# Optimization experiments

Hardware: AMD Instinct MI355X
Metric: run time of the kernel (lower is better)

The kernel has to match this reference:

```python
import jax, jax.numpy as jnp
import numpy as np

NUM_GROUPS = 32
EPS = 1e-5


def setup_inputs() -> dict:
    key = jax.random.key(0)
    ks = jax.random.split(key, 11)
    B, C, H, W = 4, 512, 64, 64
    s = 1.0 / np.sqrt(C)
    inp = {
        "x": jax.random.normal(ks[0], (B, C, H, W), dtype=jnp.float32),
        "gn_w": jnp.ones((C,), jnp.float32),
        "gn_b": jnp.zeros((C,), jnp.float32),
        "wq": jax.random.uniform(ks[1], (C, C), jnp.float32, -s, s),
        "bq": jax.random.uniform(ks[2], (C,), jnp.float32, -s, s),
        "wk": jax.random.uniform(ks[3], (C, C), jnp.float32, -s, s),
        "bk": jax.random.uniform(ks[4], (C,), jnp.float32, -s, s),
        "wv": jax.random.uniform(ks[5], (C, C), jnp.float32, -s, s),
        "bv": jax.random.uniform(ks[6], (C,), jnp.float32, -s, s),
        "wo": jax.random.uniform(ks[7], (C, C), jnp.float32, -s, s),
        "bo": jax.random.uniform(ks[8], (C,), jnp.float32, -s, s),
    }
    return inp


def reference(x, gn_w, gn_b, wq, bq, wk, bk, wv, bv, wo, bo):
    B, C, H, W = x.shape
    HW = H * W
    # GroupNorm(32, C)
    g = x.reshape(B, NUM_GROUPS, C // NUM_GROUPS, H, W)
    mu = jnp.mean(g, axis=(2, 3, 4), keepdims=True)
    var = jnp.var(g, axis=(2, 3, 4), keepdims=True)
    h = ((g - mu) * jax.lax.rsqrt(var + EPS)).reshape(B, C, H, W)
    h = h * gn_w[None, :, None, None] + gn_b[None, :, None, None]
    # Faithful to original: .view (reshape), NOT permute -> (B, HW, C)
    h = h.reshape(B, HW, C)
    q = h @ wq.T + bq  # (B, HW, C)
    k = h @ wk.T + bk
    v = h @ wv.T + bv
    # Faithful: reshape (not transpose) to (B, C, HW)
    q = q.reshape(B, C, HW)
    k = k.reshape(B, C, HW)
    v = v.reshape(B, C, HW)
    # attn: (B, HW, HW)
    attn = jnp.einsum('bcn,bcm->bnm', q, k)
    attn = jax.nn.softmax(attn, axis=-1)
    # out: (B, C, HW) = v @ attn^T
    out = jnp.einsum('bcm,bnm->bcn', v, attn)
    # transpose to (B, HW, C), out-proj, then reshape back
    out = jnp.swapaxes(out, 1, 2) @ wo.T + bo
    out = out.reshape(B, C, H, W)
    return out + x
```

## Files before the change

### kernel.cpp

```cpp
#include <hip/hip_runtime.h>
#include <hip/hip_fp16.h>
#include <math.h>

constexpr int BATCH = 4;
constexpr int HWDIM = 4096;
constexpr long CNT   = 2097152;
constexpr long ACNT  = 16777216;
constexpr int GSIZE = 65536;
constexpr float GN_EPS = 1e-5f;

typedef __attribute__((ext_vector_type(8))) _Float16 f16x8;
typedef __attribute__((ext_vector_type(4))) float f32x4;

__device__ __forceinline__ unsigned pkf16(float a, float b) {
  __half ha = __float2half(a), hb = __float2half(b);
  return (unsigned)__half_as_ushort(ha) | ((unsigned)__half_as_ushort(hb) << 16);
}
__device__ __forceinline__ float2 up2(unsigned u) {
  __half2 h = *(__half2*)&u;
  return __half22float2(h);
}
__device__ __forceinline__ void gl_lds16(const void* g, void* l) {
  __builtin_amdgcn_global_load_lds((const __attribute__((address_space(1))) unsigned*)g,
                                   (__attribute__((address_space(3))) unsigned*)l, 16, 0, 0);
}

__global__ void gn_stats_kernel(const float* __restrict__ x,
                                float* __restrict__ mu, float* __restrict__ rs) {
  const int grp = blockIdx.x;
  const float4* p = (const float4*)(x + (long)grp * GSIZE);
  float s = 0.f, q = 0.f;
  for (int i = threadIdx.x; i < GSIZE / 4; i += 256) {
    float4 v = p[i];
    s += (v.x + v.y) + (v.z + v.w);
    q += (v.x * v.x + v.y * v.y) + (v.z * v.z + v.w * v.w);
  }
  #pragma unroll
  for (int o = 32; o > 0; o >>= 1) { s += __shfl_xor(s, o, 64); q += __shfl_xor(q, o, 64); }
  __shared__ float ls[4], lq[4];
  if ((threadIdx.x & 63) == 0) { ls[threadIdx.x >> 6] = s; lq[threadIdx.x >> 6] = q; }
  __syncthreads();
  if (threadIdx.x == 0) {
    float S = (ls[0] + ls[1]) + (ls[2] + ls[3]);
    float Q = (lq[0] + lq[1]) + (lq[2] + lq[3]);
    float m = S * (1.f / GSIZE);
    float var = Q * (1.f / GSIZE) - m * m;
    mu[grp] = m; rs[grp] = rsqrtf(var + GN_EPS);
  }
}

__global__ void gn_norm_f16(const float* __restrict__ x,
                            const float* __restrict__ mu, const float* __restrict__ rs,
                            const float* __restrict__ gw, const float* __restrict__ gb,
                            unsigned short* __restrict__ h) {
  long i = ((long)blockIdx.x * 256 + threadIdx.x) * 4;
  int c   = (int)((i >> 12) & 511);
  int grp = (int)(i >> 16);
  float m = mu[grp], r = rs[grp];
  float w = gw[c] * r;
  float bia = gb[c] - m * w;
  float4 v = *(const float4*)(x + i);
  *(uint2*)(h + i) = (uint2){ pkf16(v.x * w + bia, v.y * w + bia),
                              pkf16(v.z * w + bia, v.w * w + bia) };
}

__global__ void wcvt(const float* __restrict__ w0, const float* __restrict__ w1,
                     const float* __restrict__ w2, const float* __restrict__ w3,
                     unsigned short* __restrict__ o) {
  const float* src = blockIdx.y == 0 ? w0 : blockIdx.y == 1 ? w1 : blockIdx.y == 2 ? w2 : w3;
  long e = ((long)blockIdx.x * 256 + threadIdx.x) * 4;
  float4 v = *(const float4*)(src + e);
  *(uint2*)(o + (long)blockIdx.y * 262144 + e) = (uint2){ pkf16(v.x, v.y), pkf16(v.z, v.w) };
}

template<int K>
__device__ __forceinline__ void gemm_core(const unsigned short* __restrict__ Ab, long sA,
                                          const unsigned short* __restrict__ Bb, long sB,
                                          unsigned short* LB, const int t, f32x4 (&acc)[4][4]) {
  const int lane = t & 63, w = t >> 6, wm = w & 1, wn = w >> 1;

  auto stage = [&](int buf, int k0) {
    unsigned short* S = LB + buf * 16384;
    #pragma unroll
    for (int fbi = 0; fbi < 4; fbi++) {
      int fb = w * 4 + fbi;
      int row = (fb >> 1) * 16 + (lane & 15);
      int g   = (fb & 1) * 4 + (lane >> 4);
      gl_lds16(Ab + (long)row * sA + k0 + g * 8, &S[(fb * 64) << 3]);
      gl_lds16(Bb + (long)row * sB + k0 + g * 8, &S[8192 + ((fb * 64) << 3)]);
    }
  };
  auto compute = [&](int buf) {
    const unsigned short* As = LB + buf * 16384;
    const unsigned short* Bs = As + 8192;
    #pragma unroll
    for (int kk = 0; kk < 2; kk++) {
      f16x8 a[4], b[4];
      #pragma unroll
      for (int i = 0; i < 4; i++)
        a[i] = *(const f16x8*)&As[(((wm * 4 + i) * 2 + kk) * 64 + lane) << 3];
      #pragma unroll
      for (int j = 0; j < 4; j++)
        b[j] = *(const f16x8*)&Bs[(((wn * 4 + j) * 2 + kk) * 64 + lane) << 3];
      #pragma unroll
      for (int i = 0; i < 4; i++)
        #pragma unroll
        for (int j = 0; j < 4; j++)
          acc[i][j] = __builtin_amdgcn_mfma_f32_16x16x32_f16(a[i], b[j], acc[i][j], 0, 0, 0);
    }
  };

  stage(0, 0);
  stage(1, 64);
  asm volatile("s_waitcnt vmcnt(8)" ::: "memory");
  __builtin_amdgcn_s_barrier();
  __builtin_amdgcn_sched_barrier(0);

  #pragma unroll 1
  for (int k0 = 0; k0 + 192 <= K; k0 += 64) {
    const int cur = (k0 >> 6) & 1;
    compute(cur);
    __builtin_amdgcn_sched_barrier(0);
    __builtin_amdgcn_s_barrier();
    stage(cur, k0 + 128);
    asm volatile("s_waitcnt vmcnt(8)" ::: "memory");
    __builtin_amdgcn_s_barrier();
    __builtin_amdgcn_sched_barrier(0);
  }
  compute(((K - 128) >> 6) & 1);
  asm volatile("s_waitcnt vmcnt(0)" ::: "memory");
  __builtin_amdgcn_s_barrier();
  __builtin_amdgcn_sched_barrier(0);
  compute(((K - 64) >> 6) & 1);
  __syncthreads();
}

__launch_bounds__(256)
__global__ void proj_qkv(const unsigned short* __restrict__ A, const unsigned short* __restrict__ WF,
                         const float* __restrict__ bq, const float* __restrict__ bk,
                         const float* __restrict__ bv, unsigned short* __restrict__ outq) {
  __shared__ __align__(16) unsigned short LB[32768];
  const int z = blockIdx.z;
  const unsigned short* W = WF + (long)z * 262144;
  const float* bias = z == 0 ? bq : z == 1 ? bk : bv;
  unsigned short* outp = outq + (long)z * 8388608;
  const int m0 = blockIdx.x * 128, n0 = blockIdx.y * 128;
  const int t = threadIdx.x;

  f32x4 acc[4][4];
  #pragma unroll
  for (int i = 0; i < 4; i++)
    #pragma unroll
    for (int j = 0; j < 4; j++) acc[i][j] = (f32x4){0.f, 0.f, 0.f, 0.f};

  gemm_core<512>(A + (long)m0 * 512, 512, W + (long)n0 * 512, 512, LB, t, acc);

  const int lane = t & 63, w = t >> 6, wm = w & 1, wn = w >> 1;
  const int lm = lane & 15, quad = lane >> 4;
  #pragma unroll
  for (int i = 0; i < 4; i++)
    #pragma unroll
    for (int j = 0; j < 4; j++) {
      int rr = wm * 64 + i * 16 + quad * 4;
      int cc = wn * 64 + j * 16 + lm;
      float bb = bias[n0 + cc];
      #pragma unroll
      for (int r = 0; r < 4; r++)
        LB[(rr + r) * 136 + cc] = __half_as_ushort(__float2half(acc[i][j][r] + bb));
    }
  __syncthreads();
  #pragma unroll
  for (int k = 0; k < 8; k++) {
    int ro = k * 16 + (t >> 4), col = (t & 15) * 8;
    uint4 vv = *(const uint4*)&LB[ro * 136 + col];
    *(uint4*)(outp + (long)(m0 + ro) * 512 + n0 + col) = vv;
  }
}

__launch_bounds__(256)
__global__ void proj_out(const unsigned short* __restrict__ A, const unsigned short* __restrict__ W,
                         const float* __restrict__ bias, const float* __restrict__ res,
                         float* __restrict__ outv) {
  __shared__ __align__(16) unsigned short LB[32768];
  const int m0 = blockIdx.x * 128, n0 = blockIdx.y * 128;
  const int t = threadIdx.x;

  f32x4 acc[4][4];
  #pragma unroll
  for (int i = 0; i < 4; i++)
    #pragma unroll
    for (int j = 0; j < 4; j++) acc[i][j] = (f32x4){0.f, 0.f, 0.f, 0.f};

  gemm_core<512>(A + (long)m0 * 512, 512, W + (long)n0 * 512, 512, LB, t, acc);

  const int lane = t & 63, w = t >> 6, wm = w & 1, wn = w >> 1;
  const int lm = lane & 15, quad = lane >> 4;
  #pragma unroll
  for (int i = 0; i < 4; i++)
    #pragma unroll
    for (int j = 0; j < 4; j++) {
      int nn = m0 + wm * 64 + i * 16 + quad * 4;
      int cc = n0 + wn * 64 + j * 16 + lm;
      float bb = bias[cc];
      #pragma unroll
      for (int r = 0; r < 4; r++) {
        long idx = (long)(nn + r) * 512 + cc;
        outv[idx] = acc[i][j][r] + bb + res[idx];
      }
    }
}

__global__ void transpose_f16(const unsigned short* __restrict__ qb,
                              const unsigned short* __restrict__ kb,
                              unsigned short* __restrict__ tr) {
  __shared__ __align__(16) unsigned short ld[64 * 72];
  const int zb = blockIdx.z;
  const int b = zb >> 1;
  const unsigned short* in = (zb & 1 ? kb : qb) + (long)b * CNT;
  unsigned short* o = tr + (long)b * 2 * CNT + (zb & 1 ? CNT : 0);
  const int n0 = blockIdx.x * 64, c0 = blockIdx.y * 64;
  const int t = threadIdx.x;
  unsigned* ld32 = (unsigned*)ld;
  {
    const int p = t >> 3, cg = t & 7;
    uint4 r0 = *(const uint4*)(in + (long)(c0 + 2 * p) * 4096 + n0 + 8 * cg);
    uint4 r1 = *(const uint4*)(in + (long)(c0 + 2 * p + 1) * 4096 + n0 + 8 * cg);
    unsigned aw[4] = { r0.x, r0.y, r0.z, r0.w };
    unsigned bw[4] = { r1.x, r1.y, r1.z, r1.w };
    #pragma unroll
    for (int i = 0; i < 4; i++) {
      ld32[(8 * cg + 2 * i) * 36 + p]     = (aw[i] & 0xFFFFu) | (bw[i] << 16);
      ld32[(8 * cg + 2 * i + 1) * 36 + p] = (aw[i] >> 16) | (bw[i] & 0xFFFF0000u);
    }
  }
  __syncthreads();
  {
    const int n = t >> 2, cg2 = t & 3;
    uint4 o0 = *(const uint4*)(ld + n * 72 + 16 * cg2);
    uint4 o1 = *(const uint4*)(ld + n * 72 + 16 * cg2 + 8);
    *(uint4*)(o + (long)(n0 + n) * 512 + c0 + 16 * cg2)     = o0;
    *(uint4*)(o + (long)(n0 + n) * 512 + c0 + 16 * cg2 + 8) = o1;
  }
}

__launch_bounds__(256)
__global__ void qk_f16(const unsigned short* __restrict__ tr, unsigned short* __restrict__ attn) {
  __shared__ __align__(16) unsigned short LB[32768];
  const int lin = blockIdx.x + 32 * blockIdx.y + 1024 * blockIdx.z;
  const int nl = (lin & 7) * 512 + (lin >> 3);
  const int b = nl >> 10, by = (nl >> 5) & 31, bx = nl & 31;
  const unsigned short* qT = tr + (long)b * 2 * CNT;
  const unsigned short* kT = qT + CNT;
  unsigned short* attnb = attn + (long)b * ACNT;
  const int n0 = bx * 128, m0 = by * 128;
  const int t = threadIdx.x;

  f32x4 acc[4][4];
  #pragma unroll
  for (int i = 0; i < 4; i++)
    #pragma unroll
    for (int j = 0; j < 4; j++) acc[i][j] = (f32x4){0.f, 0.f, 0.f, 0.f};

  gemm_core<512>(qT + (long)n0 * 512, 512, kT + (long)m0 * 512, 512, LB, t, acc);

  const int lane = t & 63, w = t >> 6, wm = w & 1, wn = w >> 1;
  const int lm = lane & 15, quad = lane >> 4;
  #pragma unroll
  for (int i = 0; i < 4; i++)
    #pragma unroll
    for (int j = 0; j < 4; j++) {
      int rr = wm * 64 + i * 16 + quad * 4;
      int cc = wn * 64 + j * 16 + lm;
      #pragma unroll
      for (int r = 0; r < 4; r++)
        LB[(rr + r) * 136 + cc] = __half_as_ushort(__float2half(acc[i][j][r]));
    }
  __syncthreads();
  #pragma unroll
  for (int k = 0; k < 8; k++) {
    int ro = k * 16 + (t >> 4), col = (t & 15) * 8;
    uint4 vv = *(const uint4*)&LB[ro * 136 + col];
    *(uint4*)(attnb + (long)(n0 + ro) * 4096 + m0 + col) = vv;
  }
}

__global__ void softmax_f16ip(unsigned short* __restrict__ attn) {
  unsigned short* p = attn + (long)blockIdx.x * HWDIM;
  const int t = threadIdx.x;
  uint4 u0 = *(const uint4*)(p + t * 16);
  uint4 u1 = *(const uint4*)(p + t * 16 + 8);
  float v[16];
  {
    unsigned uu[8] = { u0.x, u0.y, u0.z, u0.w, u1.x, u1.y, u1.z, u1.w };
    #pragma unroll
    for (int i = 0; i < 8; i++) { float2 f = up2(uu[i]); v[2*i] = f.x; v[2*i+1] = f.y; }
  }
  float mx = -1e30f;
  #pragma unroll
  for (int i = 0; i < 16; i++) mx = fmaxf(mx, v[i]);
  #pragma unroll
  for (int o = 32; o > 0; o >>= 1) mx = fmaxf(mx, __shfl_xor(mx, o, 64));
  __shared__ float rmax[4], rsum[4];
  if ((t & 63) == 0) rmax[t >> 6] = mx;
  __syncthreads();
  mx = fmaxf(fmaxf(rmax[0], rmax[1]), fmaxf(rmax[2], rmax[3]));
  float s = 0.f;
  #pragma unroll
  for (int i = 0; i < 16; i++) { v[i] = __expf(v[i] - mx); s += v[i]; }
  #pragma unroll
  for (int o = 32; o > 0; o >>= 1) s += __shfl_xor(s, o, 64);
  if ((t & 63) == 0) rsum[t >> 6] = s;
  __syncthreads();
  s = (rsum[0] + rsum[1]) + (rsum[2] + rsum[3]);
  float inv = 1.f / s;
  uint4 w0, w1;
  w0.x = pkf16(v[0]*inv,  v[1]*inv);  w0.y = pkf16(v[2]*inv,  v[3]*inv);
  w0.z = pkf16(v[4]*inv,  v[5]*inv);  w0.w = pkf16(v[6]*inv,  v[7]*inv);
  w1.x = pkf16(v[8]*inv,  v[9]*inv);  w1.y = pkf16(v[10]*inv, v[11]*inv);
  w1.z = pkf16(v[12]*inv, v[13]*inv); w1.w = pkf16(v[14]*inv, v[15]*inv);
  *(uint4*)(p + t * 16)     = w0;
  *(uint4*)(p + t * 16 + 8) = w1;
}

__launch_bounds__(256)
__global__ void pv_f16(const unsigned short* __restrict__ P, const unsigned short* __restrict__ V,
                       unsigned short* __restrict__ ot) {
  __shared__ __align__(16) unsigned short LB[32768];
  const int lin = blockIdx.x + 32 * blockIdx.y + 128 * blockIdx.z;
  const int nl = (lin & 7) * 64 + (lin >> 3);
  const int bx = nl & 31, by = (nl >> 5) & 3, b = nl >> 7;
  const unsigned short* Pb = P + (long)b * ACNT;
  const unsigned short* Vb = V + (long)b * CNT;
  unsigned short* Ob = ot + (long)b * CNT;
  const int n0 = bx * 128, c0 = by * 128;
  const int t = threadIdx.x;

  f32x4 acc[4][4];
  #pragma unroll
  for (int i = 0; i < 4; i++)
    #pragma unroll
    for (int j = 0; j < 4; j++) acc[i][j] = (f32x4){0.f, 0.f, 0.f, 0.f};

  gemm_core<4096>(Pb + (long)n0 * 4096, 4096, Vb + (long)c0 * 4096, 4096, LB, t, acc);

  const int lane = t & 63, w = t >> 6, wm = w & 1, wn = w >> 1;
  const int lm = lane & 15, quad = lane >> 4;
  #pragma unroll
  for (int i = 0; i < 4; i++)
    #pragma unroll
    for (int j = 0; j < 4; j++) {
      int rr = wm * 64 + i * 16 + quad * 4;
      int cc = wn * 64 + j * 16 + lm;
      #pragma unroll
      for (int r = 0; r < 4; r++)
        LB[(rr + r) * 136 + cc] = __half_as_ushort(__float2half(acc[i][j][r]));
    }
  __syncthreads();
  #pragma unroll
  for (int k = 0; k < 8; k++) {
    int ro = k * 16 + (t >> 4), col = (t & 15) * 8;
    uint4 vv = *(const uint4*)&LB[ro * 136 + col];
    *(uint4*)(Ob + (long)(n0 + ro) * 512 + c0 + col) = vv;
  }
}

extern "C" void kernel_launch(void* const* d_in, const int* in_sizes, int n_in,
                              void* d_out, int out_size, void* d_ws, size_t ws_size,
                              hipStream_t stream) {
  (void)in_sizes; (void)n_in; (void)out_size; (void)ws_size;
  const float* x  = (const float*)d_in[0];
  const float* gw = (const float*)d_in[1];
  const float* gb = (const float*)d_in[2];
  const float* wq = (const float*)d_in[3];
  const float* bq = (const float*)d_in[4];
  const float* wk = (const float*)d_in[5];
  const float* bk = (const float*)d_in[6];
  const float* wv = (const float*)d_in[7];
  const float* bv = (const float*)d_in[8];
  const float* wo = (const float*)d_in[9];
  const float* bo = (const float*)d_in[10];
  float* out = (float*)d_out;

  unsigned short* attn = (unsigned short*)d_ws;
  unsigned short* h    = attn;
  unsigned short* qf   = attn + 4 * ACNT;
  unsigned short* kf   = qf + 8388608;
  unsigned short* vf   = kf + 8388608;
  unsigned short* tr   = vf + 8388608;
  unsigned short* ot   = tr + 16777216;
  unsigned short* wf   = ot + 8388608;
  float* mu = (float*)(wf + 1048576);
  float* rs = mu + 128;

  gn_stats_kernel<<<dim3(128), dim3(256), 0, stream>>>(x, mu, rs);
  gn_norm_f16<<<dim3(8192), dim3(256), 0, stream>>>(x, mu, rs, gw, gb, h);
  wcvt<<<dim3(256, 4), dim3(256), 0, stream>>>(wq, wk, wv, wo, wf);

  proj_qkv<<<dim3(128, 4, 3), 256, 0, stream>>>(h, wf, bq, bk, bv, qf);

  transpose_f16<<<dim3(64, 8, 8), 256, 0, stream>>>(qf, kf, tr);
  qk_f16<<<dim3(32, 32, 4), 256, 0, stream>>>(tr, attn);
  softmax_f16ip<<<dim3(16384), 256, 0, stream>>>(attn);
  pv_f16<<<dim3(32, 4, 4), 256, 0, stream>>>(attn, vf, ot);

  proj_out<<<dim3(128, 4), 256, 0, stream>>>(ot, wf + 786432, bo, x, out);
}
```

Before: 512.2 us.

## Enlarge GEMM tiles to 256x256 with K=32 stages and split GroupNorm stats

```diff
diff --git a/kernel.cpp b/kernel.cpp
--- a/kernel.cpp
+++ b/kernel.cpp
@@ -24,13 +24,18 @@
   __builtin_amdgcn_global_load_lds((const __attribute__((address_space(1))) unsigned*)g,
                                    (__attribute__((address_space(3))) unsigned*)l, 16, 0, 0);
 }
-
-__global__ void gn_stats_kernel(const float* __restrict__ x,
-                                float* __restrict__ mu, float* __restrict__ rs) {
-  const int grp = blockIdx.x;
-  const float4* p = (const float4*)(x + (long)grp * GSIZE);
+template<int N> __device__ __forceinline__ void wait_vmcnt() {
+  if constexpr (N == 0)      asm volatile("s_waitcnt vmcnt(0)" ::: "memory");
+  else if constexpr (N == 4) asm volatile("s_waitcnt vmcnt(4)" ::: "memory");
+  else if constexpr (N == 6) asm volatile("s_waitcnt vmcnt(6)" ::: "memory");
+}
+
+__global__ void gn_stats_kernel(const float* __restrict__ x, float* __restrict__ sacc) {
+  const int blk = blockIdx.x;
+  const int grp = blk >> 2;
+  const float4* p = (const float4*)(x + (long)grp * GSIZE + (long)(blk & 3) * (GSIZE / 4));
   float s = 0.f, q = 0.f;
-  for (int i = threadIdx.x; i < GSIZE / 4; i += 256) {
+  for (int i = threadIdx.x; i < GSIZE / 16; i += 256) {
     float4 v = p[i];
     s += (v.x + v.y) + (v.z + v.w);
     q += (v.x * v.x + v.y * v.y) + (v.z * v.z + v.w * v.w);
@@ -41,22 +46,20 @@
   if ((threadIdx.x & 63) == 0) { ls[threadIdx.x >> 6] = s; lq[threadIdx.x >> 6] = q; }
   __syncthreads();
   if (threadIdx.x == 0) {
-    float S = (ls[0] + ls[1]) + (ls[2] + ls[3]);
-    float Q = (lq[0] + lq[1]) + (lq[2] + lq[3]);
-    float m = S * (1.f / GSIZE);
-    float var = Q * (1.f / GSIZE) - m * m;
-    mu[grp] = m; rs[grp] = rsqrtf(var + GN_EPS);
-  }
-}
-
-__global__ void gn_norm_f16(const float* __restrict__ x,
-                            const float* __restrict__ mu, const float* __restrict__ rs,
+    atomicAdd(&sacc[grp * 2],     (ls[0] + ls[1]) + (ls[2] + ls[3]));
+    atomicAdd(&sacc[grp * 2 + 1], (lq[0] + lq[1]) + (lq[2] + lq[3]));
+  }
+}
+
+__global__ void gn_norm_f16(const float* __restrict__ x, const float* __restrict__ sacc,
                             const float* __restrict__ gw, const float* __restrict__ gb,
                             unsigned short* __restrict__ h) {
   long i = ((long)blockIdx.x * 256 + threadIdx.x) * 4;
   int c   = (int)((i >> 12) & 511);
   int grp = (int)(i >> 16);
-  float m = mu[grp], r = rs[grp];
+  float S = sacc[grp * 2], Q = sacc[grp * 2 + 1];
+  float m = S * (1.f / GSIZE);
+  float r = rsqrtf(Q * (1.f / GSIZE) - m * m + GN_EPS);
   float w = gw[c] * r;
   float bia = gb[c] - m * w;
   float4 v = *(const float4*)(x + i);
@@ -73,69 +76,108 @@
   *(uint2*)(o + (long)blockIdx.y * 262144 + e) = (uint2){ pkf16(v.x, v.y), pkf16(v.z, v.w) };
 }
 
-template<int K>
+template<int BM, int BN, int NWM, int NWN, int K>
 __device__ __forceinline__ void gemm_core(const unsigned short* __restrict__ Ab, long sA,
                                           const unsigned short* __restrict__ Bb, long sB,
-                                          unsigned short* LB, const int t, f32x4 (&acc)[4][4]) {
+                                          unsigned short* LB, const int t, f32x4 (&acc)[8][4]) {
+  constexpr int NW   = NWM * NWN;
+  constexpr int APW  = BM / 16 / NW;
+  constexpr int BPW  = BN / 16 / NW;
+  constexpr int L    = APW + BPW;
+  constexpr int BUFS = (BM + BN) * 32;
   const int lane = t & 63, w = t >> 6, wm = w & 1, wn = w >> 1;
 
   auto stage = [&](int buf, int k0) {
-    unsigned short* S = LB + buf * 16384;
-    #pragma unroll
-    for (int fbi = 0; fbi < 4; fbi++) {
-      int fb = w * 4 + fbi;
-      int row = (fb >> 1) * 16 + (lane & 15);
-      int g   = (fb & 1) * 4 + (lane >> 4);
-      gl_lds16(Ab + (long)row * sA + k0 + g * 8, &S[(fb * 64) << 3]);
-      gl_lds16(Bb + (long)row * sB + k0 + g * 8, &S[8192 + ((fb * 64) << 3)]);
+    unsigned short* S = LB + buf * BUFS;
+    #pragma unroll
+    for (int i = 0; i < APW; i++) {
+      int fb = w * APW + i;
+      gl_lds16(Ab + (long)(fb * 16 + (lane & 15)) * sA + k0 + (lane >> 4) * 8, &S[fb * 512]);
+    }
+    #pragma unroll
+    for (int i = 0; i < BPW; i++) {
+      int fb = w * BPW + i;
+      gl_lds16(Bb + (long)(fb * 16 + (lane & 15)) * sB + k0 + (lane >> 4) * 8,
+               &S[BM * 32 + fb * 512]);
     }
   };
   auto compute = [&](int buf) {
-    const unsigned short* As = LB + buf * 16384;
-    const unsigned short* Bs = As + 8192;
-    #pragma unroll
-    for (int kk = 0; kk < 2; kk++) {
-      f16x8 a[4], b[4];
-      #pragma unroll
-      for (int i = 0; i < 4; i++)
-        a[i] = *(const f16x8*)&As[(((wm * 4 + i) * 2 + kk) * 64 + lane) << 3];
+    const unsigned short* As = LB + buf * BUFS;
+    const unsigned short* Bs = As + BM * 32;
+    f16x8 a[8], b[4];
+    #pragma unroll
+    for (int i = 0; i < 8; i++) a[i] = *(const f16x8*)&As[((wm * 8 + i) * 64 + lane) * 8];
+    #pragma unroll
+    for (int j = 0; j < 4; j++) b[j] = *(const f16x8*)&Bs[((wn * 4 + j) * 64 + lane) * 8];
+    #pragma unroll
+    for (int i = 0; i < 8; i++)
       #pragma unroll
       for (int j = 0; j < 4; j++)
-        b[j] = *(const f16x8*)&Bs[(((wn * 4 + j) * 2 + kk) * 64 + lane) << 3];
-      #pragma unroll
-      for (int i = 0; i < 4; i++)
-        #pragma unroll
-        for (int j = 0; j < 4; j++)
-          acc[i][j] = __builtin_amdgcn_mfma_f32_16x16x32_f16(a[i], b[j], acc[i][j], 0, 0, 0);
-    }
+        acc[i][j] = __builtin_amdgcn_mfma_f32_16x16x32_f16(a[i], b[j], acc[i][j], 0, 0, 0);
   };
 
   stage(0, 0);
-  stage(1, 64);
-  asm volatile("s_waitcnt vmcnt(8)" ::: "memory");
+  stage(1, 32);
+  wait_vmcnt<L>();
   __builtin_amdgcn_s_barrier();
   __builtin_amdgcn_sched_barrier(0);
 
   #pragma unroll 1
-  for (int k0 = 0; k0 + 192 <= K; k0 += 64) {
-    const int cur = (k0 >> 6) & 1;
+  for (int k0 = 0; k0 + 96 <= K; k0 += 32) {
+    const int cur = (k0 >> 5) & 1;
     compute(cur);
     __builtin_amdgcn_sched_barrier(0);
     __builtin_amdgcn_s_barrier();
-    stage(cur, k0 + 128);
-    asm volatile("s_waitcnt vmcnt(8)" ::: "memory");
+    stage(cur, k0 + 64);
+    wait_vmcnt<L>();
     __builtin_amdgcn_s_barrier();
     __builtin_amdgcn_sched_barrier(0);
   }
-  compute(((K - 128) >> 6) & 1);
-  asm volatile("s_waitcnt vmcnt(0)" ::: "memory");
+  compute(((K - 64) >> 5) & 1);
+  wait_vmcnt<0>();
   __builtin_amdgcn_s_barrier();
   __builtin_amdgcn_sched_barrier(0);
-  compute(((K - 64) >> 6) & 1);
-  __syncthreads();
-}
-
-__launch_bounds__(256)
+  compute(((K - 32) >> 5) & 1);
+  __syncthreads();
+}
+
+template<int BM, int BN, int NWM, int NWN>
+__device__ __forceinline__ void store_f16(unsigned short* LB, f32x4 (&acc)[8][4], const int t,
+                                          unsigned short* __restrict__ outp, long sO,
+                                          const float* __restrict__ bias) {
+  const int lane = t & 63, w = t >> 6, wm = w & 1, wn = w >> 1;
+  const int lm = lane & 15, quad = lane >> 4;
+  constexpr int TPR = BN / 8;
+  constexpr int RPR = (NWM * NWN * 64) / TPR;
+  #pragma unroll 1
+  for (int c = 0; c < BM / 64; c++) {
+    __syncthreads();
+    if (wm == (c >> 1)) {
+      #pragma unroll
+      for (int i2 = 0; i2 < 4; i2++)
+        #pragma unroll
+        for (int j = 0; j < 4; j++) {
+          int i = (c & 1) * 4 + i2;
+          int rr = i2 * 16 + quad * 4;
+          int cc = wn * 64 + j * 16 + lm;
+          float bb = bias ? bias[cc] : 0.f;
+          #pragma unroll
+          for (int r = 0; r < 4; r++)
+            LB[(rr + r) * (BN + 8) + cc] = __half_as_ushort(__float2half(acc[i][j][r] + bb));
+        }
+    }
+    __syncthreads();
+    #pragma unroll
+    for (int k = 0; k < 64 / RPR; k++) {
+      int ro = k * RPR + t / TPR;
+      int co = (t % TPR) * 8;
+      uint4 v = *(const uint4*)&LB[ro * (BN + 8) + co];
+      *(uint4*)&outp[(long)(c * 64 + ro) * sO + co] = v;
+    }
+  }
+}
+
+__launch_bounds__(512, 2)
 __global__ void proj_qkv(const unsigned short* __restrict__ A, const unsigned short* __restrict__ WF,
                          const float* __restrict__ bq, const float* __restrict__ bk,
                          const float* __restrict__ bv, unsigned short* __restrict__ outq) {
@@ -144,62 +186,42 @@
   const unsigned short* W = WF + (long)z * 262144;
   const float* bias = z == 0 ? bq : z == 1 ? bk : bv;
   unsigned short* outp = outq + (long)z * 8388608;
-  const int m0 = blockIdx.x * 128, n0 = blockIdx.y * 128;
-  const int t = threadIdx.x;
-
-  f32x4 acc[4][4];
-  #pragma unroll
-  for (int i = 0; i < 4; i++)
+  const int m0 = blockIdx.x * 256, n0 = blockIdx.y * 256;
+  const int t = threadIdx.x;
+
+  f32x4 acc[8][4];
+  #pragma unroll
+  for (int i = 0; i < 8; i++)
     #pragma unroll
     for (int j = 0; j < 4; j++) acc[i][j] = (f32x4){0.f, 0.f, 0.f, 0.f};
 
-  gemm_core<512>(A + (long)m0 * 512, 512, W + (long)n0 * 512, 512, LB, t, acc);
-
-  const int lane = t & 63, w = t >> 6, wm = w & 1, wn = w >> 1;
-  const int lm = lane & 15, quad = lane >> 4;
-  #pragma unroll
-  for (int i = 0; i < 4; i++)
-    #pragma unroll
-    for (int j = 0; j < 4; j++) {
-      int rr = wm * 64 + i * 16 + quad * 4;
-      int cc = wn * 64 + j * 16 + lm;
-      float bb = bias[n0 + cc];
-      #pragma unroll
-      for (int r = 0; r < 4; r++)
-        LB[(rr + r) * 136 + cc] = __half_as_ushort(__float2half(acc[i][j][r] + bb));
-    }
-  __syncthreads();
-  #pragma unroll
-  for (int k = 0; k < 8; k++) {
-    int ro = k * 16 + (t >> 4), col = (t & 15) * 8;
-    uint4 vv = *(const uint4*)&LB[ro * 136 + col];
-    *(uint4*)(outp + (long)(m0 + ro) * 512 + n0 + col) = vv;
-  }
-}
-
-__launch_bounds__(256)
+  gemm_core<256, 256, 2, 4, 512>(A + (long)m0 * 512, 512, W + (long)n0 * 512, 512, LB, t, acc);
+  store_f16<256, 256, 2, 4>(LB, acc, t, outp + (long)m0 * 512 + n0, 512, bias + n0);
+}
+
+__launch_bounds__(512, 2)
 __global__ void proj_out(const unsigned short* __restrict__ A, const unsigned short* __restrict__ W,
                          const float* __restrict__ bias, const float* __restrict__ res,
                          float* __restrict__ outv) {
   __shared__ __align__(16) unsigned short LB[32768];
-  const int m0 = blockIdx.x * 128, n0 = blockIdx.y * 128;
-  const int t = threadIdx.x;
-
-  f32x4 acc[4][4];
-  #pragma unroll
-  for (int i = 0; i < 4; i++)
+  const int m0 = blockIdx.x * 256, n0 = blockIdx.y * 256;
+  const int t = threadIdx.x;
+
+  f32x4 acc[8][4];
+  #pragma unroll
+  for (int i = 0; i < 8; i++)
     #pragma unroll
     for (int j = 0; j < 4; j++) acc[i][j] = (f32x4){0.f, 0.f, 0.f, 0.f};
 
-  gemm_core<512>(A + (long)m0 * 512, 512, W + (long)n0 * 512, 512, LB, t, acc);
+  gemm_core<256, 256, 2, 4, 512>(A + (long)m0 * 512, 512, W + (long)n0 * 512, 512, LB, t, acc);
 
   const int lane = t & 63, w = t >> 6, wm = w & 1, wn = w >> 1;
   const int lm = lane & 15, quad = lane >> 4;
   #pragma unroll
-  for (int i = 0; i < 4; i++)
+  for (int i = 0; i < 8; i++)
     #pragma unroll
     for (int j = 0; j < 4; j++) {
-      int nn = m0 + wm * 64 + i * 16 + quad * 4;
+      int nn = m0 + wm * 128 + i * 16 + quad * 4;
       int cc = n0 + wn * 64 + j * 16 + lm;
       float bb = bias[cc];
       #pragma unroll
@@ -243,45 +265,23 @@
   }
 }
 
-__launch_bounds__(256)
+__launch_bounds__(512, 2)
 __global__ void qk_f16(const unsigned short* __restrict__ tr, unsigned short* __restrict__ attn) {
   __shared__ __align__(16) unsigned short LB[32768];
-  const int lin = blockIdx.x + 32 * blockIdx.y + 1024 * blockIdx.z;
-  const int nl = (lin & 7) * 512 + (lin >> 3);
-  const int b = nl >> 10, by = (nl >> 5) & 31, bx = nl & 31;
+  const int b = blockIdx.z;
   const unsigned short* qT = tr + (long)b * 2 * CNT;
   const unsigned short* kT = qT + CNT;
-  unsigned short* attnb = attn + (long)b * ACNT;
-  const int n0 = bx * 128, m0 = by * 128;
-  const int t = threadIdx.x;
-
-  f32x4 acc[4][4];
-  #pragma unroll
-  for (int i = 0; i < 4; i++)
+  const int n0 = blockIdx.x * 256, m0 = blockIdx.y * 256;
+  const int t = threadIdx.x;
+
+  f32x4 acc[8][4];
+  #pragma unroll
+  for (int i = 0; i < 8; i++)
     #pragma unroll
     for (int j = 0; j < 4; j++) acc[i][j] = (f32x4){0.f, 0.f, 0.f, 0.f};
 
-  gemm_core<512>(qT + (long)n0 * 512, 512, kT + (long)m0 * 512, 512, LB, t, acc);
-
-  const int lane = t & 63, w = t >> 6, wm = w & 1, wn = w >> 1;
-  const int lm = lane & 15, quad = lane >> 4;
-  #pragma unroll
-  for (int i = 0; i < 4; i++)
-    #pragma unroll
-    for (int j = 0; j < 4; j++) {
-      int rr = wm * 64 + i * 16 + quad * 4;
-      int cc = wn * 64 + j * 16 + lm;
-      #pragma unroll
-      for (int r = 0; r < 4; r++)
-        LB[(rr + r) * 136 + cc] = __half_as_ushort(__float2half(acc[i][j][r]));
-    }
-  __syncthreads();
-  #pragma unroll
-  for (int k = 0; k < 8; k++) {
-    int ro = k * 16 + (t >> 4), col = (t & 15) * 8;
-    uint4 vv = *(const uint4*)&LB[ro * 136 + col];
-    *(uint4*)(attnb + (long)(n0 + ro) * 4096 + m0 + col) = vv;
-  }
+  gemm_core<256, 256, 2, 4, 512>(qT + (long)n0 * 512, 512, kT + (long)m0 * 512, 512, LB, t, acc);
+  store_f16<256, 256, 2, 4>(LB, acc, t, attn + (long)b * ACNT + (long)n0 * 4096 + m0, 4096, nullptr);
 }
 
 __global__ void softmax_f16ip(unsigned short* __restrict__ attn) {
@@ -322,46 +322,25 @@
   *(uint4*)(p + t * 16 + 8) = w1;
 }
 
-__launch_bounds__(256)
+__launch_bounds__(256, 2)
 __global__ void pv_f16(const unsigned short* __restrict__ P, const unsigned short* __restrict__ V,
                        unsigned short* __restrict__ ot) {
-  __shared__ __align__(16) unsigned short LB[32768];
-  const int lin = blockIdx.x + 32 * blockIdx.y + 128 * blockIdx.z;
-  const int nl = (lin & 7) * 64 + (lin >> 3);
-  const int bx = nl & 31, by = (nl >> 5) & 3, b = nl >> 7;
+  __shared__ __align__(16) unsigned short LB[24576];
+  const int b = blockIdx.z;
   const unsigned short* Pb = P + (long)b * ACNT;
   const unsigned short* Vb = V + (long)b * CNT;
   unsigned short* Ob = ot + (long)b * CNT;
-  const int n0 = bx * 128, c0 = by * 128;
-  const int t = threadIdx.x;
-
-  f32x4 acc[4][4];
-  #pragma unroll
-  for (int i = 0; i < 4; i++)
+  const int n0 = blockIdx.x * 256, c0 = blockIdx.y * 128;
+  const int t = threadIdx.x;
+
+  f32x4 acc[8][4];
+  #pragma unroll
+  for (int i = 0; i < 8; i++)
     #pragma unroll
     for (int j = 0; j < 4; j++) acc[i][j] = (f32x4){0.f, 0.f, 0.f, 0.f};
 
-  gemm_core<4096>(Pb + (long)n0 * 4096, 4096, Vb + (long)c0 * 4096, 4096, LB, t, acc);
-
-  const int lane = t & 63, w = t >> 6, wm = w & 1, wn = w >> 1;
-  const int lm = lane & 15, quad = lane >> 4;
-  #pragma unroll
-  for (int i = 0; i < 4; i++)
-    #pragma unroll
-    for (int j = 0; j < 4; j++) {
-      int rr = wm * 64 + i * 16 + quad * 4;
-      int cc = wn * 64 + j * 16 + lm;
-      #pragma unroll
-      for (int r = 0; r < 4; r++)
-        LB[(rr + r) * 136 + cc] = __half_as_ushort(__float2half(acc[i][j][r]));
-    }
-  __syncthreads();
-  #pragma unroll
-  for (int k = 0; k < 8; k++) {
-    int ro = k * 16 + (t >> 4), col = (t & 15) * 8;
-    uint4 vv = *(const uint4*)&LB[ro * 136 + col];
-    *(uint4*)(Ob + (long)(n0 + ro) * 512 + c0 + col) = vv;
-  }
+  gemm_core<256, 128, 2, 2, 4096>(Pb + (long)n0 * 4096, 4096, Vb + (long)c0 * 4096, 4096, LB, t, acc);
+  store_f16<256, 128, 2, 2>(LB, acc, t, Ob + (long)n0 * 512 + c0, 512, nullptr);
 }
 
 extern "C" void kernel_launch(void* const* d_in, const int* in_sizes, int n_in,
@@ -389,19 +368,19 @@
   unsigned short* tr   = vf + 8388608;
   unsigned short* ot   = tr + 16777216;
   unsigned short* wf   = ot + 8388608;
-  float* mu = (float*)(wf + 1048576);
-  float* rs = mu + 128;
-
-  gn_stats_kernel<<<dim3(128), dim3(256), 0, stream>>>(x, mu, rs);
-  gn_norm_f16<<<dim3(8192), dim3(256), 0, stream>>>(x, mu, rs, gw, gb, h);
+  float* sacc = (float*)(wf + 1048576);
+
+  hipMemsetAsync(sacc, 0, 256 * sizeof(float), stream);
+  gn_stats_kernel<<<dim3(512), dim3(256), 0, stream>>>(x, sacc);
+  gn_norm_f16<<<dim3(8192), dim3(256), 0, stream>>>(x, sacc, gw, gb, h);
   wcvt<<<dim3(256, 4), dim3(256), 0, stream>>>(wq, wk, wv, wo, wf);
 
-  proj_qkv<<<dim3(128, 4, 3), 256, 0, stream>>>(h, wf, bq, bk, bv, qf);
+  proj_qkv<<<dim3(64, 2, 3), 512, 0, stream>>>(h, wf, bq, bk, bv, qf);
 
   transpose_f16<<<dim3(64, 8, 8), 256, 0, stream>>>(qf, kf, tr);
-  qk_f16<<<dim3(32, 32, 4), 256, 0, stream>>>(tr, attn);
+  qk_f16<<<dim3(16, 16, 4), 512, 0, stream>>>(tr, attn);
   softmax_f16ip<<<dim3(16384), 256, 0, stream>>>(attn);
-  pv_f16<<<dim3(32, 4, 4), 256, 0, stream>>>(attn, vf, ot);
-
-  proj_out<<<dim3(128, 4), 256, 0, stream>>>(ot, wf + 786432, bo, x, out);
-}
+  pv_f16<<<dim3(16, 4, 4), 256, 0, stream>>>(attn, vf, ot);
+
+  proj_out<<<dim3(64, 2), 512, 0, stream>>>(ot, wf + 786432, bo, x, out);
+}
```

New measurement: 647.0 us. +26.3%, slower.
